# Performance work log

Hardware: AMD Instinct MI355X
Metric: run time of the kernel (lower is better)

The kernel has to match this reference:

```python
import jax, jax.numpy as jnp
import numpy as np

NEG_INF = -9e15
ALPHA = 0.2  # LeakyReLU negative slope

N = 8192
D_IN = 512
D_OUT = 256


def setup_inputs() -> dict:
    key = jax.random.key(0)
    k1, k2, k3, k4, k5 = jax.random.split(key, 5)
    features = jax.random.normal(k1, (N, D_IN), dtype=jnp.float32)
    adjacency_matrix = jax.random.randint(k2, (N, N), 0, 2, dtype=jnp.int32)
    # learned params (torch Linear stores [out, in]; we use [in, out] layout)
    s_phi = 1.0 / np.sqrt(D_IN)
    W_phi = jax.random.uniform(k3, (D_IN, D_OUT), jnp.float32, -s_phi, s_phi)
    s_v = 1.0 / np.sqrt(D_OUT)
    w_mu = jax.random.uniform(k4, (D_OUT,), jnp.float32, -s_v, s_v)
    w_xi = jax.random.uniform(k5, (D_OUT,), jnp.float32, -s_v, s_v)
    return {"features": features, "adjacency_matrix": adjacency_matrix,
            "W_phi": W_phi, "w_mu": w_mu, "w_xi": w_xi}


def reference(features, adjacency_matrix, W_phi, w_mu, w_xi):
    h = features @ W_phi                                   # [N, d_out]
    mu = h @ w_mu                                          # [N]
    xi = h @ w_xi                                          # [N]
    e = mu[:, None] + xi[None, :]                          # [N, N] additive scores
    e = jnp.where(e >= 0, e, ALPHA * e)                    # LeakyReLU
    e = jnp.where(adjacency_matrix > 0, e, NEG_INF)        # mask non-edges
    a = jax.nn.softmax(e, axis=1)                          # row softmax (dropout p=0)
    out = a @ h                                            # weighted aggregation
    return jax.nn.elu(out)
```

## Files before the change

### kernel.cpp

```cpp
#include <hip/hip_runtime.h>
#include <cstdint>
#include <cstddef>


#define LOG2E 1.44269504f

typedef __attribute__((ext_vector_type(8))) short short8;
typedef __attribute__((ext_vector_type(4))) float floatx4;

using uint_as1 = __attribute__((address_space(1))) unsigned int;
using uint_as3 = __attribute__((address_space(3))) unsigned int;

__device__ __forceinline__ void gld_lds16(const void* g, void* l) {
  __builtin_amdgcn_global_load_lds((const uint_as1*)g, (uint_as3*)l, 16, 0, 0);
}

__device__ __forceinline__ unsigned short f2b(float f) {
  unsigned u = __float_as_uint(f);
  u += 0x7fffu + ((u >> 16) & 1u);
  return (unsigned short)(u >> 16);
}
__device__ __forceinline__ float b2f(short s) {
  return __uint_as_float(((unsigned)(unsigned short)s) << 16);
}

__global__ void k_bitmask(const int* __restrict__ adj, unsigned long long* __restrict__ bm) {
  int gw = (blockIdx.x * 256 + threadIdx.x) >> 6;
  int lane = threadIdx.x & 63;
  size_t w0 = (size_t)gw * 128;
  for (int r = 0; r < 128; r += 4) {
    size_t wd = w0 + r;
    int v0 = adj[(wd + 0) * 64 + lane];
    int v1 = adj[(wd + 1) * 64 + lane];
    int v2 = adj[(wd + 2) * 64 + lane];
    int v3 = adj[(wd + 3) * 64 + lane];
    unsigned long long m0 = __ballot(v0 != 0);
    unsigned long long m1 = __ballot(v1 != 0);
    unsigned long long m2 = __ballot(v2 != 0);
    unsigned long long m3 = __ballot(v3 != 0);
    if (lane == 0) {
      bm[wd] = m0; bm[wd + 1] = m1; bm[wd + 2] = m2; bm[wd + 3] = m3;
    }
  }
}

__global__ void k_cvt_features(const float* __restrict__ f, unsigned short* __restrict__ fb) {
  int tid = blockIdx.x * 256 + threadIdx.x;
  float4 v = ((const float4*)f)[tid];
  ushort4 o = {f2b(v.x), f2b(v.y), f2b(v.z), f2b(v.w)};
  *(ushort4*)&fb[tid * 4] = o;
}

__global__ void k_prep_wt(const float* __restrict__ w, unsigned short* __restrict__ wt) {
  int tid = blockIdx.x * 256 + threadIdx.x;
  int n = tid >> 9, k = tid & 511;
  wt[n * 512 + k] = f2b(w[k * 256 + n]);
}

__global__ void k_prep_p(const float* __restrict__ w, const float* __restrict__ wmu,
                         const float* __restrict__ wxi, float* __restrict__ pmu,
                         float* __restrict__ pxi) {
  int tid = blockIdx.x * 256 + threadIdx.x;
  int k = tid >> 2, seg = tid & 3;
  float sm = 0.f, sx = 0.f;
  int base = k * 256 + seg * 64;
#pragma unroll
  for (int c = 0; c < 64; c += 4) {
    float4 wv = *(const float4*)&w[base + c];
    float4 mv = *(const float4*)&wmu[seg * 64 + c];
    float4 xv = *(const float4*)&wxi[seg * 64 + c];
    sm += wv.x * mv.x + wv.y * mv.y + wv.z * mv.z + wv.w * mv.w;
    sx += wv.x * xv.x + wv.y * xv.y + wv.z * xv.z + wv.w * xv.w;
  }
  sm += __shfl_xor(sm, 1); sm += __shfl_xor(sm, 2);
  sx += __shfl_xor(sx, 1); sx += __shfl_xor(sx, 2);
  if (seg == 0) { pmu[k] = sm; pxi[k] = sx; }
}

__global__ void k_mu_xi(const unsigned short* __restrict__ fb, const float* __restrict__ pmu,
                        const float* __restrict__ pxi, float* __restrict__ Emu,
                        float* __restrict__ Fmu, float* __restrict__ Exi,
                        float* __restrict__ Fxi) {
  int w = threadIdx.x >> 6, l = threadIdx.x & 63;
  int i = blockIdx.x * 4 + w;
  short8 fv = *(const short8*)&fb[i * 512 + l * 8];
  float m = 0.f, x = 0.f;
#pragma unroll
  for (int c = 0; c < 8; ++c) {
    float fvf = b2f(fv[c]);
    m = fmaf(fvf, pmu[l * 8 + c], m);
    x = fmaf(fvf, pxi[l * 8 + c], x);
  }
#pragma unroll
  for (int off = 32; off > 0; off >>= 1) {
    m += __shfl_xor(m, off);
    x += __shfl_xor(x, off);
  }
  if (l == 0) {
    float ms = m * LOG2E, xs = x * LOG2E;
    Emu[i] = __builtin_amdgcn_exp2f(ms);
    Fmu[i] = __builtin_amdgcn_exp2f(0.2f * ms);
    Exi[i] = __builtin_amdgcn_exp2f(xs);
    Fxi[i] = __builtin_amdgcn_exp2f(0.2f * xs);
  }
}

__global__ __launch_bounds__(256, 2) void k_gemm1(const unsigned short* __restrict__ fb,
                                                  const unsigned short* __restrict__ wt,
                                                  unsigned short* __restrict__ ht) {
  __shared__ __align__(16) unsigned short As[64 * 64];
  __shared__ __align__(16) unsigned short Bs[128 * 64];
  int t = threadIdx.x, w = t >> 6, l = t & 63;
  int bm_ = blockIdx.x >> 1, bn = blockIdx.x & 1;
  int m0 = bm_ * 64, n0 = bn * 128;
  int lr = l >> 3, lg = l & 7, g = lg ^ lr;
  int kg = l >> 4, ln = l & 15;
  floatx4 zero = {0.f, 0.f, 0.f, 0.f};
  floatx4 acc[4][2];
#pragma unroll
  for (int mf = 0; mf < 4; ++mf)
#pragma unroll
    for (int nf = 0; nf < 2; ++nf) acc[mf][nf] = zero;

  for (int it = 0; it < 8; ++it) {
    int k0 = it * 64;
#pragma unroll
    for (int q = 0; q < 2; ++q) {
      int row = w * 16 + q * 8 + lr;
      const void* gp = fb + (size_t)(m0 + row) * 512 + k0 + g * 8;
      int lb = __builtin_amdgcn_readfirstlane((w * 16 + q * 8) * 64);
      gld_lds16(gp, &As[lb]);
    }
#pragma unroll
    for (int q = 0; q < 4; ++q) {
      int row = w * 32 + q * 8 + lr;
      const void* gp = wt + (size_t)(n0 + row) * 512 + k0 + g * 8;
      int lb = __builtin_amdgcn_readfirstlane((w * 32 + q * 8) * 64);
      gld_lds16(gp, &Bs[lb]);
    }
    __syncthreads();
#pragma unroll
    for (int ks = 0; ks < 2; ++ks) {
      int gg = ks * 4 + kg;
      int swz = (gg ^ (ln & 7)) * 8;
      short8 bfr[2];
#pragma unroll
      for (int nf = 0; nf < 2; ++nf)
        bfr[nf] = *(const short8*)&Bs[(w * 32 + nf * 16 + ln) * 64 + swz];
#pragma unroll
      for (int mf = 0; mf < 4; ++mf) {
        short8 afr = *(const short8*)&As[(mf * 16 + ln) * 64 + swz];
#pragma unroll
        for (int nf = 0; nf < 2; ++nf)
          acc[mf][nf] = __builtin_amdgcn_mfma_f32_16x16x32_bf16(afr, bfr[nf], acc[mf][nf], 0, 0, 0);
      }
    }
    __syncthreads();
  }
#pragma unroll
  for (int mf = 0; mf < 4; ++mf)
#pragma unroll
    for (int nf = 0; nf < 2; ++nf) {
      int ng = n0 + w * 32 + nf * 16 + ln;
      int mg = m0 + mf * 16 + kg * 4;
      ushort4 o = {f2b(acc[mf][nf][0]), f2b(acc[mf][nf][1]),
                   f2b(acc[mf][nf][2]), f2b(acc[mf][nf][3])};
      *(ushort4*)&ht[(size_t)ng * 8192 + mg] = o;
    }
}

__global__ __launch_bounds__(256, 2) void k_attn6(const unsigned char* __restrict__ bm8,
                                                  const unsigned short* __restrict__ ht,
                                                  const float* __restrict__ Emu,
                                                  const float* __restrict__ Fmu,
                                                  const float* __restrict__ Exi,
                                                  const float* __restrict__ Fxi,
                                                  float* __restrict__ nump,
                                                  float* __restrict__ zpart) {
  __shared__ __align__(16) unsigned short Bs[128 * 256];
  __shared__ __align__(16) unsigned char BitS[256 * 32];
  __shared__ __align__(16) float ExiS[256];
  __shared__ __align__(16) float FxiS[256];

  int t = threadIdx.x, w = t >> 6, l = t & 63;
  int ln = l & 15, kg = l >> 4;
  int b = blockIdx.x;
  int ib = b & 31, nb = (b >> 5) & 1, jb = b >> 6;
  int i0 = ib * 256, n0 = nb * 128;
  int jbase = jb * 1024;

  float emu[4], fmu[4];
#pragma unroll
  for (int mf = 0; mf < 4; ++mf) {
    int i = i0 + w * 64 + mf * 16 + ln;
    emu[mf] = Emu[i];
    fmu[mf] = Fmu[i];
  }

  floatx4 zero = {0.f, 0.f, 0.f, 0.f};
  floatx4 acc[4][8];
#pragma unroll
  for (int mf = 0; mf < 4; ++mf)
#pragma unroll
    for (int nf = 0; nf < 8; ++nf) acc[mf][nf] = zero;
  floatx4 accz[4];
#pragma unroll
  for (int mf = 0; mf < 4; ++mf) accz[mf] = zero;

  short8 ones;
#pragma unroll
  for (int e = 0; e < 8; ++e) ones[e] = (short)0x3F80;

  for (int win = 0; win < 4; ++win) {
    int jcol = jbase + win * 256;
    __syncthreads();
#pragma unroll
    for (int q = 0; q < 16; ++q) {
      int r0 = w * 32 + q * 2;
      int rowl = r0 + (l >> 5);
      int glog = (l & 31) ^ (rowl & 7);
      const void* gp = ht + (size_t)(n0 + rowl) * 8192 + jcol + glog * 8;
      int lb = __builtin_amdgcn_readfirstlane(r0 * 256);
      gld_lds16(gp, &Bs[lb]);
    }
#pragma unroll
    for (int q2 = 0; q2 < 2; ++q2) {
      int r0 = w * 64 + q2 * 32;
      int row = r0 + (l >> 1);
      const void* gp = bm8 + (size_t)(i0 + row) * 1024 + (jcol >> 3) + (l & 1) * 16;
      int lb = __builtin_amdgcn_readfirstlane(r0 * 32);
      gld_lds16(gp, &BitS[lb]);
    }
    if (w == 2) gld_lds16(Exi + jcol + l * 4, &ExiS[0]);
    if (w == 3) gld_lds16(Fxi + jcol + l * 4, &FxiS[0]);
    __syncthreads();

#pragma unroll
    for (int ks = 0; ks < 8; ++ks) {
      int gran = ks * 4 + kg;
      int jo = gran * 8;
      float4 e0 = *(const float4*)&ExiS[jo];
      float4 e1 = *(const float4*)&ExiS[jo + 4];
      float4 f0 = *(const float4*)&FxiS[jo];
      float4 f1 = *(const float4*)&FxiS[jo + 4];
      float ex[8] = {e0.x, e0.y, e0.z, e0.w, e1.x, e1.y, e1.z, e1.w};
      float fx[8] = {f0.x, f0.y, f0.z, f0.w, f1.x, f1.y, f1.z, f1.w};
      short8 af[4];
#pragma unroll
      for (int mf = 0; mf < 4; ++mf) {
        unsigned bits = BitS[(w * 64 + mf * 16 + ln) * 32 + gran];
        float A = emu[mf], F = fmu[mf];
#pragma unroll
        for (int e = 0; e < 8; ++e) {
          float wv = fmaxf(A * ex[e], F * fx[e]);
          wv = (bits & (1u << e)) ? wv : 0.f;
          af[mf][e] = (short)f2b(wv);
        }
      }
#pragma unroll
      for (int mf = 0; mf < 4; ++mf)
        accz[mf] = __builtin_amdgcn_mfma_f32_16x16x32_bf16(af[mf], ones, accz[mf], 0, 0, 0);
#pragma unroll
      for (int nf = 0; nf < 8; ++nf) {
        int nl = nf * 16 + ln;
        short8 bf = *(const short8*)&Bs[nl * 256 + ((gran ^ (nl & 7)) * 8)];
#pragma unroll
        for (int mf = 0; mf < 4; ++mf)
          acc[mf][nf] = __builtin_amdgcn_mfma_f32_16x16x32_bf16(af[mf], bf, acc[mf][nf], 0, 0, 0);
      }
    }
  }

  float* np = nump + (size_t)jb * (8192 * 256);
#pragma unroll
  for (int mf = 0; mf < 4; ++mf) {
    int rowb = i0 + w * 64 + mf * 16 + kg * 4;
#pragma unroll
    for (int nf = 0; nf < 8; ++nf) {
      int col = n0 + nf * 16 + ln;
#pragma unroll
      for (int r = 0; r < 4; ++r)
        np[(size_t)(rowb + r) * 256 + col] = acc[mf][nf][r];
    }
    if (nb == 0 && ln == 0) {
#pragma unroll
      for (int r = 0; r < 4; ++r)
        zpart[jb * 8192 + rowb + r] = accz[mf][r];
    }
  }
}

__global__ void k_final(const float* __restrict__ nump, const float* __restrict__ zpart,
                        float* __restrict__ out) {
  int tid = blockIdx.x * 256 + threadIdx.x;
  int i = tid >> 6;
  float z = 0.f;
#pragma unroll
  for (int p = 0; p < 8; ++p) z += zpart[p * 8192 + i];
  float zi = 1.0f / z;
  float4 v = {0.f, 0.f, 0.f, 0.f};
#pragma unroll
  for (int p = 0; p < 8; ++p) {
    float4 s = *(const float4*)&nump[(size_t)p * (8192 * 256) + tid * 4];
    v.x += s.x; v.y += s.y; v.z += s.z; v.w += s.w;
  }
  v.x *= zi; v.y *= zi; v.z *= zi; v.w *= zi;
  v.x = (v.x > 0.f) ? v.x : (__builtin_amdgcn_exp2f(v.x * LOG2E) - 1.f);
  v.y = (v.y > 0.f) ? v.y : (__builtin_amdgcn_exp2f(v.y * LOG2E) - 1.f);
  v.z = (v.z > 0.f) ? v.z : (__builtin_amdgcn_exp2f(v.z * LOG2E) - 1.f);
  v.w = (v.w > 0.f) ? v.w : (__builtin_amdgcn_exp2f(v.w * LOG2E) - 1.f);
  *(float4*)&out[tid * 4] = v;
}

extern "C" void kernel_launch(void* const* d_in, const int* in_sizes, int n_in,
                              void* d_out, int out_size, void* d_ws, size_t ws_size,
                              hipStream_t stream) {
  const float* features = (const float*)d_in[0];
  const int* adjm = (const int*)d_in[1];
  const float* W_phi = (const float*)d_in[2];
  const float* w_mu = (const float*)d_in[3];
  const float* w_xi = (const float*)d_in[4];
  float* out = (float*)d_out;

  char* ws = (char*)d_ws;
  unsigned short* fb  = (unsigned short*)(ws + 0);
  unsigned short* ht  = (unsigned short*)(ws + 8388608);
  unsigned short* wt  = (unsigned short*)(ws + 12582912);
  float* pmu = (float*)(ws + 12845056);
  float* pxi = (float*)(ws + 12847104);
  float* Emu = (float*)(ws + 12849152);
  float* Fmu = (float*)(ws + 12881920);
  float* Exi = (float*)(ws + 12914688);
  float* Fxi = (float*)(ws + 12947456);
  unsigned char* bmask = (unsigned char*)(ws + 13631488);
  float* zpart = (float*)(ws + 22020096);
  float* nump  = (float*)(ws + 25165824);

  k_bitmask<<<2048, 256, 0, stream>>>(adjm, (unsigned long long*)bmask);
  k_cvt_features<<<4096, 256, 0, stream>>>(features, fb);
  k_prep_wt<<<512, 256, 0, stream>>>(W_phi, wt);
  k_prep_p<<<8, 256, 0, stream>>>(W_phi, w_mu, w_xi, pmu, pxi);
  k_mu_xi<<<2048, 256, 0, stream>>>(fb, pmu, pxi, Emu, Fmu, Exi, Fxi);
  k_gemm1<<<256, 256, 0, stream>>>(fb, wt, ht);
  k_attn6<<<512, 256, 0, stream>>>(bmask, ht, Emu, Fmu, Exi, Fxi, nump, zpart);
  k_final<<<2048, 256, 0, stream>>>(nump, zpart, out);
}
```

Before: 497.9 us.

## Materialize bf16 attention weight matrix then run plain GEMM for aggregation

Replaces the bitmask precompute and the fused weight-generation-plus-MFMA attention kernel with two stages. The first stage reads adjacency directly, writes a dense bf16 weight matrix and computes fp32 row sums. The second stage is a pure tiled bf16 GEMM against ht. This removes the per-tile VALU weight generation, which the old kernel duplicated across the two column halves, from the matrix-core loop. In exchange it adds a large round-trip of the N×N weight matrix through global memory and re-reads ht far more often.

```diff
diff --git a/kernel.cpp b/kernel.cpp
--- a/kernel.cpp
+++ b/kernel.cpp
@@ -22,26 +22,6 @@
 }
 __device__ __forceinline__ float b2f(short s) {
   return __uint_as_float(((unsigned)(unsigned short)s) << 16);
-}
-
-__global__ void k_bitmask(const int* __restrict__ adj, unsigned long long* __restrict__ bm) {
-  int gw = (blockIdx.x * 256 + threadIdx.x) >> 6;
-  int lane = threadIdx.x & 63;
-  size_t w0 = (size_t)gw * 128;
-  for (int r = 0; r < 128; r += 4) {
-    size_t wd = w0 + r;
-    int v0 = adj[(wd + 0) * 64 + lane];
-    int v1 = adj[(wd + 1) * 64 + lane];
-    int v2 = adj[(wd + 2) * 64 + lane];
-    int v3 = adj[(wd + 3) * 64 + lane];
-    unsigned long long m0 = __ballot(v0 != 0);
-    unsigned long long m1 = __ballot(v1 != 0);
-    unsigned long long m2 = __ballot(v2 != 0);
-    unsigned long long m3 = __ballot(v3 != 0);
-    if (lane == 0) {
-      bm[wd] = m0; bm[wd + 1] = m1; bm[wd + 2] = m2; bm[wd + 3] = m3;
-    }
-  }
 }
 
 __global__ void k_cvt_features(const float* __restrict__ f, unsigned short* __restrict__ fb) {
@@ -169,135 +149,131 @@
     }
 }
 
-__global__ __launch_bounds__(256, 2) void k_attn6(const unsigned char* __restrict__ bm8,
-                                                  const unsigned short* __restrict__ ht,
-                                                  const float* __restrict__ Emu,
-                                                  const float* __restrict__ Fmu,
-                                                  const float* __restrict__ Exi,
-                                                  const float* __restrict__ Fxi,
-                                                  float* __restrict__ nump,
-                                                  float* __restrict__ zpart) {
-  __shared__ __align__(16) unsigned short Bs[128 * 256];
-  __shared__ __align__(16) unsigned char BitS[256 * 32];
-  __shared__ __align__(16) float ExiS[256];
-  __shared__ __align__(16) float FxiS[256];
-
+__global__ __launch_bounds__(256, 4) void k_wmat(const int* __restrict__ adj,
+                                                 const float* __restrict__ Emu,
+                                                 const float* __restrict__ Fmu,
+                                                 const float* __restrict__ Exi,
+                                                 const float* __restrict__ Fxi,
+                                                 unsigned short* __restrict__ W,
+                                                 float* __restrict__ zbuf) {
+  int w = threadIdx.x >> 6, l = threadIdx.x & 63;
+  int i = blockIdx.x * 4 + w;
+  float EM = Emu[i], FM = Fmu[i];
+  const int* arow = adj + (size_t)i * 8192;
+  unsigned short* wrow = W + (size_t)i * 8192;
+  float zacc = 0.f;
+#pragma unroll 2
+  for (int it = 0; it < 8; ++it) {
+    int j = it * 1024 + l * 16;
+    const int4* ap = (const int4*)(arow + j);
+    int4 a0 = ap[0], a1 = ap[1], a2 = ap[2], a3 = ap[3];
+    float4 e0 = *(const float4*)&Exi[j];
+    float4 e1 = *(const float4*)&Exi[j + 4];
+    float4 e2 = *(const float4*)&Exi[j + 8];
+    float4 e3 = *(const float4*)&Exi[j + 12];
+    float4 f0 = *(const float4*)&Fxi[j];
+    float4 f1 = *(const float4*)&Fxi[j + 4];
+    float4 f2 = *(const float4*)&Fxi[j + 8];
+    float4 f3 = *(const float4*)&Fxi[j + 12];
+    int am[16] = {a0.x, a0.y, a0.z, a0.w, a1.x, a1.y, a1.z, a1.w,
+                  a2.x, a2.y, a2.z, a2.w, a3.x, a3.y, a3.z, a3.w};
+    float ex[16] = {e0.x, e0.y, e0.z, e0.w, e1.x, e1.y, e1.z, e1.w,
+                    e2.x, e2.y, e2.z, e2.w, e3.x, e3.y, e3.z, e3.w};
+    float fx[16] = {f0.x, f0.y, f0.z, f0.w, f1.x, f1.y, f1.z, f1.w,
+                    f2.x, f2.y, f2.z, f2.w, f3.x, f3.y, f3.z, f3.w};
+    short8 p0, p1;
+#pragma unroll
+    for (int e = 0; e < 16; ++e) {
+      float wv = fmaxf(EM * ex[e], FM * fx[e]);
+      wv = (am[e] != 0) ? wv : 0.f;
+      zacc += wv;
+      if (e < 8) p0[e] = (short)f2b(wv); else p1[e - 8] = (short)f2b(wv);
+    }
+    *(short8*)&wrow[j] = p0;
+    *(short8*)&wrow[j + 8] = p1;
+  }
+#pragma unroll
+  for (int off = 32; off > 0; off >>= 1) zacc += __shfl_xor(zacc, off);
+  if (l == 0) zbuf[i] = zacc;
+}
+
+__global__ __launch_bounds__(256, 3) void k_gatt(const unsigned short* __restrict__ W,
+                                                 const unsigned short* __restrict__ ht,
+                                                 float* __restrict__ nump) {
+  __shared__ __align__(16) unsigned short Ws[64 * 64];
+  __shared__ __align__(16) unsigned short Bs[256 * 64];
   int t = threadIdx.x, w = t >> 6, l = t & 63;
   int ln = l & 15, kg = l >> 4;
-  int b = blockIdx.x;
-  int ib = b & 31, nb = (b >> 5) & 1, jb = b >> 6;
-  int i0 = ib * 256, n0 = nb * 128;
-  int jbase = jb * 1024;
-
-  float emu[4], fmu[4];
+  int lr = l >> 3, g = (l & 7) ^ lr;
+  int ib = blockIdx.x & 127, jb = blockIdx.x >> 7;
+  int i0 = ib * 64;
+  size_t jwin = (size_t)jb * 1024;
+
+  floatx4 zero = {0.f, 0.f, 0.f, 0.f};
+  floatx4 acc[4][4];
+#pragma unroll
+  for (int mf = 0; mf < 4; ++mf)
+#pragma unroll
+    for (int nf = 0; nf < 4; ++nf) acc[mf][nf] = zero;
+
+  const unsigned short* wbase = W + (size_t)i0 * 8192 + jwin;
+  const unsigned short* hbase = ht + jwin;
+
+  for (int c = 0; c < 16; ++c) {
+    int jo = c * 64;
+#pragma unroll
+    for (int q = 0; q < 2; ++q) {
+      int r0 = w * 16 + q * 8;
+      const void* gp = wbase + (size_t)(r0 + lr) * 8192 + jo + g * 8;
+      int lb = __builtin_amdgcn_readfirstlane(r0 * 64);
+      gld_lds16(gp, &Ws[lb]);
+    }
+#pragma unroll
+    for (int q = 0; q < 8; ++q) {
+      int r0 = w * 64 + q * 8;
+      const void* gp = hbase + (size_t)(r0 + lr) * 8192 + jo + g * 8;
+      int lb = __builtin_amdgcn_readfirstlane(r0 * 64);
+      gld_lds16(gp, &Bs[lb]);
+    }
+    __syncthreads();
+#pragma unroll
+    for (int ks = 0; ks < 2; ++ks) {
+      int swz = ((ks * 4 + kg) ^ (ln & 7)) * 8;
+      short8 af[4], bf[4];
+#pragma unroll
+      for (int mf = 0; mf < 4; ++mf)
+        af[mf] = *(const short8*)&Ws[(mf * 16 + ln) * 64 + swz];
+#pragma unroll
+      for (int nf = 0; nf < 4; ++nf)
+        bf[nf] = *(const short8*)&Bs[(w * 64 + nf * 16 + ln) * 64 + swz];
+#pragma unroll
+      for (int mf = 0; mf < 4; ++mf)
+#pragma unroll
+        for (int nf = 0; nf < 4; ++nf)
+          acc[mf][nf] = __builtin_amdgcn_mfma_f32_16x16x32_bf16(af[mf], bf[nf], acc[mf][nf], 0, 0, 0);
+    }
+    __syncthreads();
+  }
+
+  float* np = nump + (size_t)jb * (8192 * 256);
 #pragma unroll
   for (int mf = 0; mf < 4; ++mf) {
-    int i = i0 + w * 64 + mf * 16 + ln;
-    emu[mf] = Emu[i];
-    fmu[mf] = Fmu[i];
-  }
-
-  floatx4 zero = {0.f, 0.f, 0.f, 0.f};
-  floatx4 acc[4][8];
-#pragma unroll
-  for (int mf = 0; mf < 4; ++mf)
-#pragma unroll
-    for (int nf = 0; nf < 8; ++nf) acc[mf][nf] = zero;
-  floatx4 accz[4];
-#pragma unroll
-  for (int mf = 0; mf < 4; ++mf) accz[mf] = zero;
-
-  short8 ones;
-#pragma unroll
-  for (int e = 0; e < 8; ++e) ones[e] = (short)0x3F80;
-
-  for (int win = 0; win < 4; ++win) {
-    int jcol = jbase + win * 256;
-    __syncthreads();
-#pragma unroll
-    for (int q = 0; q < 16; ++q) {
-      int r0 = w * 32 + q * 2;
-      int rowl = r0 + (l >> 5);
-      int glog = (l & 31) ^ (rowl & 7);
-      const void* gp = ht + (size_t)(n0 + rowl) * 8192 + jcol + glog * 8;
-      int lb = __builtin_amdgcn_readfirstlane(r0 * 256);
-      gld_lds16(gp, &Bs[lb]);
-    }
-#pragma unroll
-    for (int q2 = 0; q2 < 2; ++q2) {
-      int r0 = w * 64 + q2 * 32;
-      int row = r0 + (l >> 1);
-      const void* gp = bm8 + (size_t)(i0 + row) * 1024 + (jcol >> 3) + (l & 1) * 16;
-      int lb = __builtin_amdgcn_readfirstlane(r0 * 32);
-      gld_lds16(gp, &BitS[lb]);
-    }
-    if (w == 2) gld_lds16(Exi + jcol + l * 4, &ExiS[0]);
-    if (w == 3) gld_lds16(Fxi + jcol + l * 4, &FxiS[0]);
-    __syncthreads();
-
-#pragma unroll
-    for (int ks = 0; ks < 8; ++ks) {
-      int gran = ks * 4 + kg;
-      int jo = gran * 8;
-      float4 e0 = *(const float4*)&ExiS[jo];
-      float4 e1 = *(const float4*)&ExiS[jo + 4];
-      float4 f0 = *(const float4*)&FxiS[jo];
-      float4 f1 = *(const float4*)&FxiS[jo + 4];
-      float ex[8] = {e0.x, e0.y, e0.z, e0.w, e1.x, e1.y, e1.z, e1.w};
-      float fx[8] = {f0.x, f0.y, f0.z, f0.w, f1.x, f1.y, f1.z, f1.w};
-      short8 af[4];
-#pragma unroll
-      for (int mf = 0; mf < 4; ++mf) {
-        unsigned bits = BitS[(w * 64 + mf * 16 + ln) * 32 + gran];
-        float A = emu[mf], F = fmu[mf];
-#pragma unroll
-        for (int e = 0; e < 8; ++e) {
-          float wv = fmaxf(A * ex[e], F * fx[e]);
-          wv = (bits & (1u << e)) ? wv : 0.f;
-          af[mf][e] = (short)f2b(wv);
-        }
-      }
-#pragma unroll
-      for (int mf = 0; mf < 4; ++mf)
-        accz[mf] = __builtin_amdgcn_mfma_f32_16x16x32_bf16(af[mf], ones, accz[mf], 0, 0, 0);
-#pragma unroll
-      for (int nf = 0; nf < 8; ++nf) {
-        int nl = nf * 16 + ln;
-        short8 bf = *(const short8*)&Bs[nl * 256 + ((gran ^ (nl & 7)) * 8)];
-#pragma unroll
-        for (int mf = 0; mf < 4; ++mf)
-          acc[mf][nf] = __builtin_amdgcn_mfma_f32_16x16x32_bf16(af[mf], bf, acc[mf][nf], 0, 0, 0);
-      }
-    }
-  }
-
-  float* np = nump + (size_t)jb * (8192 * 256);
-#pragma unroll
-  for (int mf = 0; mf < 4; ++mf) {
-    int rowb = i0 + w * 64 + mf * 16 + kg * 4;
-#pragma unroll
-    for (int nf = 0; nf < 8; ++nf) {
-      int col = n0 + nf * 16 + ln;
+    int rowb = i0 + mf * 16 + kg * 4;
+#pragma unroll
+    for (int nf = 0; nf < 4; ++nf) {
+      int col = w * 64 + nf * 16 + ln;
 #pragma unroll
       for (int r = 0; r < 4; ++r)
         np[(size_t)(rowb + r) * 256 + col] = acc[mf][nf][r];
     }
-    if (nb == 0 && ln == 0) {
-#pragma unroll
-      for (int r = 0; r < 4; ++r)
-        zpart[jb * 8192 + rowb + r] = accz[mf][r];
-    }
-  }
-}
-
-__global__ void k_final(const float* __restrict__ nump, const float* __restrict__ zpart,
+  }
+}
+
+__global__ void k_final(const float* __restrict__ nump, const float* __restrict__ zbuf,
                         float* __restrict__ out) {
   int tid = blockIdx.x * 256 + threadIdx.x;
   int i = tid >> 6;
-  float z = 0.f;
-#pragma unroll
-  for (int p = 0; p < 8; ++p) z += zpart[p * 8192 + i];
-  float zi = 1.0f / z;
+  float zi = 1.0f / zbuf[i];
   float4 v = {0.f, 0.f, 0.f, 0.f};
 #pragma unroll
   for (int p = 0; p < 8; ++p) {
@@ -332,16 +308,16 @@
   float* Fmu = (float*)(ws + 12881920);
   float* Exi = (float*)(ws + 12914688);
   float* Fxi = (float*)(ws + 12947456);
-  unsigned char* bmask = (unsigned char*)(ws + 13631488);
-  float* zpart = (float*)(ws + 22020096);
-  float* nump  = (float*)(ws + 25165824);
-
-  k_bitmask<<<2048, 256, 0, stream>>>(adjm, (unsigned long long*)bmask);
+  float* zbuf = (float*)(ws + 12980224);
+  unsigned short* Wm = (unsigned short*)(ws + 16777216);
+  float* nump = (float*)(ws + 150994944);
+
   k_cvt_features<<<4096, 256, 0, stream>>>(features, fb);
   k_prep_wt<<<512, 256, 0, stream>>>(W_phi, wt);
   k_prep_p<<<8, 256, 0, stream>>>(W_phi, w_mu, w_xi, pmu, pxi);
   k_mu_xi<<<2048, 256, 0, stream>>>(fb, pmu, pxi, Emu, Fmu, Exi, Fxi);
   k_gemm1<<<256, 256, 0, stream>>>(fb, wt, ht);
-  k_attn6<<<512, 256, 0, stream>>>(bmask, ht, Emu, Fmu, Exi, Fxi, nump, zpart);
-  k_final<<<2048, 256, 0, stream>>>(nump, zpart, out);
-}
+  k_wmat<<<2048, 256, 0, stream>>>(adjm, Emu, Fmu, Exi, Fxi, Wm, zbuf);
+  k_gatt<<<1024, 256, 0, stream>>>(Wm, ht, nump);
+  k_final<<<2048, 256, 0, stream>>>(nump, zbuf, out);
+}
```

Result: slower. 529.0 us (+6.2%).

## Compute full 256-column output per block to avoid recomputing attention weights

Applied to the files above, without the earlier changes.

The attention kernel now has each block cover all 256 output features instead of splitting them across two blocks. This halves the recomputation of masked attention weights and of the bitmask loads. The four waves are arranged 2x2 (rows x columns), each holding a 128x128 accumulator tile. bf16 conversion becomes plain truncation packed two values per word, and the LDS swizzle widens to 32 granules. The cost is double the LDS for the B tile, many more accumulator registers (occupancy 1), and only 256 blocks in the grid.

```diff
diff --git a/kernel.cpp b/kernel.cpp
--- a/kernel.cpp
+++ b/kernel.cpp
@@ -169,7 +169,7 @@
     }
 }
 
-__global__ __launch_bounds__(256, 2) void k_attn6(const unsigned char* __restrict__ bm8,
+__global__ __launch_bounds__(256, 1) void k_gatt2(const unsigned char* __restrict__ bm8,
                                                   const unsigned short* __restrict__ ht,
                                                   const float* __restrict__ Emu,
                                                   const float* __restrict__ Fmu,
@@ -177,49 +177,49 @@
                                                   const float* __restrict__ Fxi,
                                                   float* __restrict__ nump,
                                                   float* __restrict__ zpart) {
-  __shared__ __align__(16) unsigned short Bs[128 * 256];
+  __shared__ __align__(16) unsigned short Bs[256 * 256];
   __shared__ __align__(16) unsigned char BitS[256 * 32];
   __shared__ __align__(16) float ExiS[256];
   __shared__ __align__(16) float FxiS[256];
 
   int t = threadIdx.x, w = t >> 6, l = t & 63;
-  int ln = l & 15, kg = l >> 4;
-  int b = blockIdx.x;
-  int ib = b & 31, nb = (b >> 5) & 1, jb = b >> 6;
-  int i0 = ib * 256, n0 = nb * 128;
-  int jbase = jb * 1024;
-
-  float emu[4], fmu[4];
-#pragma unroll
-  for (int mf = 0; mf < 4; ++mf) {
-    int i = i0 + w * 64 + mf * 16 + ln;
-    emu[mf] = Emu[i];
-    fmu[mf] = Fmu[i];
+  int ln = l & 15, kg = l >> 4, kg8 = kg * 8;
+  int wi = w >> 1, wn = w & 1;
+  int jb = blockIdx.x & 7, ig = blockIdx.x >> 3;
+  int i0 = ig * 256;
+  int jw0 = jb * 1024;
+
+  float EM[8], FM[8];
+#pragma unroll
+  for (int mf = 0; mf < 8; ++mf) {
+    int i = i0 + wi * 128 + mf * 16 + ln;
+    EM[mf] = Emu[i];
+    FM[mf] = Fmu[i];
   }
 
   floatx4 zero = {0.f, 0.f, 0.f, 0.f};
-  floatx4 acc[4][8];
-#pragma unroll
-  for (int mf = 0; mf < 4; ++mf)
+  floatx4 acc[8][8];
+#pragma unroll
+  for (int mf = 0; mf < 8; ++mf)
 #pragma unroll
     for (int nf = 0; nf < 8; ++nf) acc[mf][nf] = zero;
-  floatx4 accz[4];
-#pragma unroll
-  for (int mf = 0; mf < 4; ++mf) accz[mf] = zero;
+  floatx4 accz[8];
+#pragma unroll
+  for (int mf = 0; mf < 8; ++mf) accz[mf] = zero;
 
   short8 ones;
 #pragma unroll
   for (int e = 0; e < 8; ++e) ones[e] = (short)0x3F80;
 
   for (int win = 0; win < 4; ++win) {
-    int jcol = jbase + win * 256;
+    int jc = jw0 + win * 256;
     __syncthreads();
 #pragma unroll
-    for (int q = 0; q < 16; ++q) {
-      int r0 = w * 32 + q * 2;
-      int rowl = r0 + (l >> 5);
-      int glog = (l & 31) ^ (rowl & 7);
-      const void* gp = ht + (size_t)(n0 + rowl) * 8192 + jcol + glog * 8;
+    for (int q = 0; q < 32; ++q) {
+      int r0 = w * 64 + q * 2;
+      int row = r0 + (l >> 5);
+      int g = (l & 31) ^ (row & 31);
+      const void* gp = ht + (size_t)row * 8192 + jc + g * 8;
       int lb = __builtin_amdgcn_readfirstlane(r0 * 256);
       gld_lds16(gp, &Bs[lb]);
     }
@@ -227,62 +227,65 @@
     for (int q2 = 0; q2 < 2; ++q2) {
       int r0 = w * 64 + q2 * 32;
       int row = r0 + (l >> 1);
-      const void* gp = bm8 + (size_t)(i0 + row) * 1024 + (jcol >> 3) + (l & 1) * 16;
+      const void* gp = bm8 + (size_t)(i0 + row) * 1024 + jb * 128 + win * 32 + (l & 1) * 16;
       int lb = __builtin_amdgcn_readfirstlane(r0 * 32);
       gld_lds16(gp, &BitS[lb]);
     }
-    if (w == 2) gld_lds16(Exi + jcol + l * 4, &ExiS[0]);
-    if (w == 3) gld_lds16(Fxi + jcol + l * 4, &FxiS[0]);
+    if (w == 2) gld_lds16(Exi + jc + l * 4, &ExiS[0]);
+    if (w == 3) gld_lds16(Fxi + jc + l * 4, &FxiS[0]);
     __syncthreads();
 
 #pragma unroll
     for (int ks = 0; ks < 8; ++ks) {
       int gran = ks * 4 + kg;
-      int jo = gran * 8;
-      float4 e0 = *(const float4*)&ExiS[jo];
-      float4 e1 = *(const float4*)&ExiS[jo + 4];
-      float4 f0 = *(const float4*)&FxiS[jo];
-      float4 f1 = *(const float4*)&FxiS[jo + 4];
+      float4 e0 = *(const float4*)&ExiS[gran * 8];
+      float4 e1 = *(const float4*)&ExiS[gran * 8 + 4];
+      float4 f0 = *(const float4*)&FxiS[gran * 8];
+      float4 f1 = *(const float4*)&FxiS[gran * 8 + 4];
       float ex[8] = {e0.x, e0.y, e0.z, e0.w, e1.x, e1.y, e1.z, e1.w};
       float fx[8] = {f0.x, f0.y, f0.z, f0.w, f1.x, f1.y, f1.z, f1.w};
-      short8 af[4];
-#pragma unroll
-      for (int mf = 0; mf < 4; ++mf) {
-        unsigned bits = BitS[(w * 64 + mf * 16 + ln) * 32 + gran];
-        float A = emu[mf], F = fmu[mf];
+      short8 bfv[8];
+#pragma unroll
+      for (int nf = 0; nf < 8; ++nf) {
+        int n = wn * 128 + nf * 16 + ln;
+        bfv[nf] = *(const short8*)&Bs[n * 256 + ((gran ^ (n & 31)) * 8)];
+      }
+#pragma unroll
+      for (int mf = 0; mf < 8; ++mf) {
+        unsigned bits = BitS[(wi * 128 + mf * 16 + ln) * 32 + gran];
+        float A = EM[mf], F = FM[mf];
+        float vv[8];
 #pragma unroll
         for (int e = 0; e < 8; ++e) {
-          float wv = fmaxf(A * ex[e], F * fx[e]);
-          wv = (bits & (1u << e)) ? wv : 0.f;
-          af[mf][e] = (short)f2b(wv);
+          float m = fmaxf(A * ex[e], F * fx[e]);
+          vv[e] = (bits & (1u << e)) ? m : 0.f;
         }
+        union { uint4 u; short8 s; } cv;
+        cv.u.x = (__float_as_uint(vv[1]) & 0xFFFF0000u) | (__float_as_uint(vv[0]) >> 16);
+        cv.u.y = (__float_as_uint(vv[3]) & 0xFFFF0000u) | (__float_as_uint(vv[2]) >> 16);
+        cv.u.z = (__float_as_uint(vv[5]) & 0xFFFF0000u) | (__float_as_uint(vv[4]) >> 16);
+        cv.u.w = (__float_as_uint(vv[7]) & 0xFFFF0000u) | (__float_as_uint(vv[6]) >> 16);
+        short8 af = cv.s;
+        accz[mf] = __builtin_amdgcn_mfma_f32_16x16x32_bf16(af, ones, accz[mf], 0, 0, 0);
+#pragma unroll
+        for (int nf = 0; nf < 8; ++nf)
+          acc[mf][nf] = __builtin_amdgcn_mfma_f32_16x16x32_bf16(af, bfv[nf], acc[mf][nf], 0, 0, 0);
       }
-#pragma unroll
-      for (int mf = 0; mf < 4; ++mf)
-        accz[mf] = __builtin_amdgcn_mfma_f32_16x16x32_bf16(af[mf], ones, accz[mf], 0, 0, 0);
-#pragma unroll
-      for (int nf = 0; nf < 8; ++nf) {
-        int nl = nf * 16 + ln;
-        short8 bf = *(const short8*)&Bs[nl * 256 + ((gran ^ (nl & 7)) * 8)];
-#pragma unroll
-        for (int mf = 0; mf < 4; ++mf)
-          acc[mf][nf] = __builtin_amdgcn_mfma_f32_16x16x32_bf16(af[mf], bf, acc[mf][nf], 0, 0, 0);
-      }
     }
   }
 
   float* np = nump + (size_t)jb * (8192 * 256);
 #pragma unroll
-  for (int mf = 0; mf < 4; ++mf) {
-    int rowb = i0 + w * 64 + mf * 16 + kg * 4;
-#pragma unroll
-    for (int nf = 0; nf < 8; ++nf) {
-      int col = n0 + nf * 16 + ln;
-#pragma unroll
-      for (int r = 0; r < 4; ++r)
-        np[(size_t)(rowb + r) * 256 + col] = acc[mf][nf][r];
-    }
-    if (nb == 0 && ln == 0) {
+  for (int mf = 0; mf < 8; ++mf) {
+    int rowb = i0 + wi * 128 + mf * 16 + kg * 4;
+#pragma unroll
+    for (int r = 0; r < 4; ++r) {
+      float* rp = np + (size_t)(rowb + r) * 256 + wn * 128;
+#pragma unroll
+      for (int nf = 0; nf < 8; ++nf)
+        rp[nf * 16 + ln] = acc[mf][nf][r];
+    }
+    if (wn == 0 && ln == 0) {
 #pragma unroll
       for (int r = 0; r < 4; ++r)
         zpart[jb * 8192 + rowb + r] = accz[mf][r];
@@ -342,6 +345,6 @@
   k_prep_p<<<8, 256, 0, stream>>>(W_phi, w_mu, w_xi, pmu, pxi);
   k_mu_xi<<<2048, 256, 0, stream>>>(fb, pmu, pxi, Emu, Fmu, Exi, Fxi);
   k_gemm1<<<256, 256, 0, stream>>>(fb, wt, ht);
-  k_attn6<<<512, 256, 0, stream>>>(bmask, ht, Emu, Fmu, Exi, Fxi, nump, zpart);
+  k_gatt2<<<256, 256, 0, stream>>>(bmask, ht, Emu, Fmu, Exi, Fxi, nump, zpart);
   k_final<<<2048, 256, 0, stream>>>(nump, zpart, out);
 }
```

After: 555.5 us. +11.6%, slower.
